# Kernel tuning notes

Measured on AMD Instinct MI355X. Metric: run time of the kernel, lower is better.

The kernel has to match this reference:

```python
import jax, jax.numpy as jnp
import numpy as np

B, T, C = 1, 2048, 2048
N_HEAD, N_KV = 32, 8
HD = C // N_HEAD            # 64
N_REP = N_HEAD // N_KV      # 4
WINDOW = 512                # sliding_window
N_GLOBAL = 16               # n_global_tokens


def setup_inputs() -> dict:
    key = jax.random.key(0)
    ks = jax.random.split(key, 5)
    x = jax.random.normal(ks[0], (B, T, C), jnp.float32)
    # standard RoPE frequency tables, shape (T, HD//2)
    inv_freq = 1.0 / (10000.0 ** (np.arange(0, HD, 2, dtype=np.float32) / HD))
    ang = np.outer(np.arange(T, dtype=np.float32), inv_freq)
    freqs_cos = jnp.asarray(np.cos(ang), jnp.float32)
    freqs_sin = jnp.asarray(np.sin(ang), jnp.float32)
    s = 0.02
    wq = jax.random.normal(ks[1], (C, C), jnp.float32) * s
    wk = jax.random.normal(ks[2], (N_KV * HD, C), jnp.float32) * s
    wv = jax.random.normal(ks[3], (N_KV * HD, C), jnp.float32) * s
    wo = jax.random.normal(ks[4], (C, C), jnp.float32) * s
    return {"x": x, "freqs_cos": freqs_cos, "freqs_sin": freqs_sin,
            "wq": wq, "wk": wk, "wv": wv, "wo": wo}


def _apply_rope(xh, fc, fs):
    # xh: (B, H, T, HD); fc/fs: (T, HD//2) broadcast over (B, H)
    xr = xh.reshape(*xh.shape[:-1], HD // 2, 2)
    x0, x1 = xr[..., 0], xr[..., 1]
    fc = fc[None, None]
    fs = fs[None, None]
    out = jnp.stack([x0 * fc - x1 * fs, x0 * fs + x1 * fc], axis=-1)
    return out.reshape(xh.shape)


def reference(x, freqs_cos, freqs_sin, wq, wk, wv, wo):
    Bx, Tx, Cx = x.shape
    q = (x @ wq.T).reshape(Bx, Tx, N_HEAD, HD).transpose(0, 2, 1, 3)   # (B,Hq,T,hd)
    k = (x @ wk.T).reshape(Bx, Tx, N_KV, HD).transpose(0, 2, 1, 3)     # (B,Hkv,T,hd)
    v = (x @ wv.T).reshape(Bx, Tx, N_KV, HD).transpose(0, 2, 1, 3)
    q = _apply_rope(q, freqs_cos, freqs_sin)
    k = _apply_rope(k, freqs_cos, freqs_sin)

    # GQA: group query heads over shared kv heads instead of repeat_kv
    qg = q.reshape(Bx, N_KV, N_REP, Tx, HD)
    scale = 1.0 / float(np.sqrt(HD))
    scores = jnp.einsum('bgrqd,bgkd->bgrqk', qg, k) * scale  # (B,G,R,T,T)

    # sliding-window causal mask with global tokens (kv_cache=None branch)
    q_pos = jnp.arange(Tx)[:, None]
    k_pos = jnp.arange(Tx)[None, :]
    mask = (k_pos <= q_pos) & (k_pos >= q_pos - (WINDOW - 1))
    mask = mask | (k_pos < N_GLOBAL)
    # note: global columns combined with causal rows always leave >=1 valid key
    scores = jnp.where(mask[None, None, None], scores, -jnp.inf)
    probs = jax.nn.softmax(scores, axis=-1)

    y = jnp.einsum('bgrqk,bgkd->bgrqd', probs, v)
    y = y.reshape(Bx, N_HEAD, Tx, HD).transpose(0, 2, 1, 3).reshape(Bx, Tx, Cx)
    return y @ wo.T  # dropout p=0 in eval
```

## Files before the change

### kernel.cpp

```cpp
#include <hip/hip_runtime.h>
#include <hip/hip_bf16.h>

using short4v = __attribute__((ext_vector_type(4))) short;
using short8 = __attribute__((ext_vector_type(8))) short;
using f32x4  = __attribute__((ext_vector_type(4))) float;
using f32x16 = __attribute__((ext_vector_type(16))) float;
using int4v  = __attribute__((ext_vector_type(4))) int;

#define T_SEQ  2048
#define C_DIM  2048
#define NH     32
#define NKV    8
#define HD     64
#define WINDOW 512
#define NGLOB  16
#define KLOG   0.180336880f

__device__ inline ushort f2bf(float f) {
  union { float f; unsigned u; } v; v.f = f;
  unsigned u = v.u;
  u += 0x7fffu + ((u >> 16) & 1u);
  return (ushort)(u >> 16);
}
__device__ inline float bf2f(ushort h) {
  union { unsigned u; float f; } v; v.u = ((unsigned)h) << 16;
  return v.f;
}
__device__ inline float max3f(float a, float b, float c) { return fmaxf(fmaxf(a, b), c); }

__device__ __forceinline__ void gl_lds16(const ushort* g, ushort* l) {
  __builtin_amdgcn_global_load_lds(
      (const __attribute__((address_space(1))) void*)g,
      (__attribute__((address_space(3))) void*)l, 16, 0, 0);
}

__device__ __forceinline__ f32x16 zero16() {
  f32x16 v;
#pragma unroll
  for (int i = 0; i < 16; i++) v[i] = 0.f;
  return v;
}

__device__ __forceinline__ short8 cvt8(f32x4 a, f32x4 b) {
  unsigned w0, w1, w2, w3;
  asm("v_cvt_pk_bf16_f32 %0, %1, %2" : "=v"(w0) : "v"(a[0]), "v"(a[1]));
  asm("v_cvt_pk_bf16_f32 %0, %1, %2" : "=v"(w1) : "v"(a[2]), "v"(a[3]));
  asm("v_cvt_pk_bf16_f32 %0, %1, %2" : "=v"(w2) : "v"(b[0]), "v"(b[1]));
  asm("v_cvt_pk_bf16_f32 %0, %1, %2" : "=v"(w3) : "v"(b[2]), "v"(b[3]));
  int4v w = { (int)w0, (int)w1, (int)w2, (int)w3 };
  return __builtin_bit_cast(short8, w);
}

__global__ void cvt_all(const float* __restrict__ s0, ushort* __restrict__ d0, int n0,
                        const float* __restrict__ s1, ushort* __restrict__ d1, int n1,
                        const float* __restrict__ s2, ushort* __restrict__ d2, int n2,
                        const float* __restrict__ s3, ushort* __restrict__ d3, int n3,
                        const float* __restrict__ s4, ushort* __restrict__ d4, int n4) {
  int total = n0 + n1 + n2 + n3 + n4;
  int stride = gridDim.x * blockDim.x;
  for (int i = blockIdx.x * blockDim.x + threadIdx.x; i < total; i += stride) {
    int j = i; const float* s; ushort* d;
    if (j < n0) { s = s0; d = d0; }
    else { j -= n0;
      if (j < n1) { s = s1; d = d1; }
      else { j -= n1;
        if (j < n2) { s = s2; d = d2; }
        else { j -= n2;
          if (j < n3) { s = s3; d = d3; }
          else { j -= n3; s = s4; d = d4; } } } }
    f32x4 a = *reinterpret_cast<const f32x4*>(s + (size_t)j * 8);
    f32x4 b = *reinterpret_cast<const f32x4*>(s + (size_t)j * 8 + 4);
    *reinterpret_cast<short8*>(d + (size_t)j * 8) = cvt8(a, b);
  }
}

template <int MODE>
__global__ __launch_bounds__(256) void gemm2p(const ushort* __restrict__ A,
                                              const ushort* __restrict__ B0,
                                              const ushort* __restrict__ B1,
                                              const ushort* __restrict__ B2,
                                              void* __restrict__ C0,
                                              void* __restrict__ C1,
                                              void* __restrict__ C2,
                                              const float* __restrict__ fc,
                                              const float* __restrict__ fs,
                                              int K) {
  __shared__ ushort As[2][2][128][32];
  __shared__ ushort Bs[2][2][64][32];
  const int tid  = threadIdx.x;
  const int lane = tid & 63;
  const int wid  = tid >> 6;
  const int wr = wid >> 1, wc = wid & 1;
  const int r16 = lane & 15, g16 = (lane >> 4) & 3;

  int id = blockIdx.x + blockIdx.y * gridDim.x;
  int c8 = id & 7, rr = id >> 3;
  int bx, by;
  if constexpr (MODE == 1) { bx = (c8 & 3) * 12 + (rr % 12); by = (c8 >> 2) * 8 + rr / 12; }
  else                     { bx = (c8 & 3) * 8  + (rr % 8);  by = (c8 >> 2) * 8 + rr / 8; }

  const ushort* Brow;
  void* Cout;
  int ldc, col0;
  bool vtr = false;
  if constexpr (MODE == 1) {
    if (bx < 32)      { Brow = B0 + (size_t)bx * 64 * K;        Cout = C0; ldc = 2048; col0 = bx * 64; }
    else if (bx < 40) { Brow = B1 + (size_t)(bx - 32) * 64 * K; Cout = C1; ldc = 512;  col0 = (bx - 32) * 64; }
    else              { Brow = B2 + (size_t)(bx - 40) * 64 * K; Cout = C2; ldc = 512;  col0 = (bx - 40) * 64; vtr = true; }
  } else {
    Brow = B0 + (size_t)bx * 64 * K; Cout = C0; ldc = 2048; col0 = bx * 64;
  }
  const ushort* Arow = A + (size_t)by * 128 * K;

  f32x4 acc[4][2];
#pragma unroll
  for (int i = 0; i < 4; i++)
#pragma unroll
    for (int j = 0; j < 2; j++) acc[i][j] = (f32x4){0.f, 0.f, 0.f, 0.f};

  const int srow = tid >> 2, scch = tid & 3;
  const int ssc  = scch ^ ((srow >> 1) & 3);
  const int rchunk = (g16 ^ ((r16 >> 1) & 3)) * 8;

  const int nt = K >> 6;
  int d = 0;

#define STAGE(dd, k0)                                                               \
  {                                                                                 \
    gl_lds16(&Arow[(size_t)srow * K + (k0) + ssc * 8],             &As[dd][0][srow][scch * 8]);      \
    gl_lds16(&Arow[(size_t)(srow + 64) * K + (k0) + ssc * 8],      &As[dd][0][srow + 64][scch * 8]); \
    gl_lds16(&Arow[(size_t)srow * K + (k0) + 32 + ssc * 8],        &As[dd][1][srow][scch * 8]);      \
    gl_lds16(&Arow[(size_t)(srow + 64) * K + (k0) + 32 + ssc * 8], &As[dd][1][srow + 64][scch * 8]); \
    gl_lds16(&Brow[(size_t)srow * K + (k0) + ssc * 8],             &Bs[dd][0][srow][scch * 8]);      \
    gl_lds16(&Brow[(size_t)srow * K + (k0) + 32 + ssc * 8],        &Bs[dd][1][srow][scch * 8]);      \
  }

  STAGE(0, 0);
  __syncthreads();

  for (int t = 0; t < nt; ++t) {
    if (t + 1 < nt) STAGE(d ^ 1, (t + 1) * 64);
#pragma unroll
    for (int kk = 0; kk < 2; kk++) {
      short8 af[4], bfv[2];
#pragma unroll
      for (int i = 0; i < 4; i++)
        af[i] = *reinterpret_cast<const short8*>(&As[d][kk][wr * 64 + i * 16 + r16][rchunk]);
#pragma unroll
      for (int j = 0; j < 2; j++)
        bfv[j] = *reinterpret_cast<const short8*>(&Bs[d][kk][wc * 32 + j * 16 + r16][rchunk]);
#pragma unroll
      for (int i = 0; i < 4; i++)
#pragma unroll
        for (int j = 0; j < 2; j++)
          acc[i][j] = __builtin_amdgcn_mfma_f32_16x16x32_bf16(af[i], bfv[j], acc[i][j], 0, 0, 0);
    }
    __syncthreads();
    d ^= 1;
  }
#undef STAGE

  const bool doRope = (MODE == 1) && !vtr;
  const float ksc = (MODE == 1 && bx < 32) ? KLOG : 1.0f;

#pragma unroll
  for (int i = 0; i < 4; i++)
#pragma unroll
    for (int j = 0; j < 2; j++) {
      int col = col0 + wc * 32 + j * 16 + r16;
      int row0 = by * 128 + wr * 64 + i * 16 + g16 * 4;
      if (MODE == 1 && vtr) {
        short4v tv;
#pragma unroll
        for (int r = 0; r < 4; r++) tv[r] = (short)f2bf(acc[i][j][r]);
        *reinterpret_cast<short4v*>(&((ushort*)Cout)[(size_t)col * T_SEQ + row0]) = tv;
      } else if (doRope) {
        int pr = (col & 63) >> 1;
        bool ev = ((col & 1) == 0);
#pragma unroll
        for (int r = 0; r < 4; r++) {
          float a = acc[i][j][r];
          float b = __shfl_xor(a, 1);
          int t = row0 + r;
          float cv = fc[t * 32 + pr], sv = fs[t * 32 + pr];
          float v = ev ? (a * cv - b * sv) : (b * sv + a * cv);
          ((ushort*)Cout)[(size_t)t * ldc + col] = f2bf(v * ksc);
        }
      } else {
#pragma unroll
        for (int r = 0; r < 4; r++) {
          if constexpr (MODE == 0) ((float*)Cout)[(size_t)(row0 + r) * ldc + col] = acc[i][j][r];
          else                     ((ushort*)Cout)[(size_t)(row0 + r) * ldc + col] = f2bf(acc[i][j][r]);
        }
      }
    }
}

__global__ __launch_bounds__(512) void attn32(const ushort* __restrict__ Q,
                                              const ushort* __restrict__ K,
                                              const ushort* __restrict__ Vt,
                                              ushort* __restrict__ Y) {
  __shared__ ushort Klds[2][2][2048];
  __shared__ ushort Vlds[2][2][2048];
  __shared__ float oS[4][64][33];
  __shared__ float mS[4][32];
  __shared__ float sS[4][64];
  ushort (*Ot)[32][72] = reinterpret_cast<ushort (*)[32][72]>(&oS[0][0][0]);
  const int tid  = threadIdx.x;
  const int lane = tid & 63;
  const int wv   = tid >> 6;
  const int hh   = wv & 3;
  const int split = wv >> 2;
  const int g  = blockIdx.x & 7;
  const int qt = 63 - (blockIdx.x >> 3);
  const int h  = g * 4 + hh;
  const int q0 = qt << 5;
  const int l31 = lane & 31, hi = lane >> 5;
  const int hi8 = hi << 3, hi4 = hi << 2;
  const int qrow = q0 + l31;

  short8 qf[4];
#pragma unroll
  for (int s = 0; s < 4; s++)
    qf[s] = *reinterpret_cast<const short8*>(&Q[(size_t)qrow * C_DIM + h * HD + s * 16 + hi8]);

  f32x16 o[2] = { zero16(), zero16() };
  f32x16 sacc = zero16();
  float mrow = -1e30f;
  short8 ones8;
#pragma unroll
  for (int s = 0; s < 8; s++) ones8[s] = (short)0x3F80;

  auto pack8 = [&](const float* pp) -> short8 {
    unsigned wA, wB, wC, wD;
    asm("v_cvt_pk_bf16_f32 %0, %1, %2" : "=v"(wA) : "v"(pp[0]), "v"(pp[1]));
    asm("v_cvt_pk_bf16_f32 %0, %1, %2" : "=v"(wB) : "v"(pp[2]), "v"(pp[3]));
    asm("v_cvt_pk_bf16_f32 %0, %1, %2" : "=v"(wC) : "v"(pp[4]), "v"(pp[5]));
    asm("v_cvt_pk_bf16_f32 %0, %1, %2" : "=v"(wD) : "v"(pp[6]), "v"(pp[7]));
    asm("v_permlane32_swap_b32 %0, %1" : "+v"(wA), "+v"(wC));
    asm("v_permlane32_swap_b32 %0, %1" : "+v"(wB), "+v"(wD));
    int4v w4 = { (int)wA, (int)wB, (int)wC, (int)wD };
    return __builtin_bit_cast(short8, w4);
  };

  int wsr = (q0 - (WINDOW - 1)) >> 5;
  int wstart = (wsr < 1) ? 32 : (wsr << 5);
  int ntw = (q0 >= wstart) ? (((q0 - wstart) >> 5) + 1) : 0;
  const int NT = 1 + ntw;
  const int ihalf = (NT + 1) >> 1;

#define KBOF(i) ((i) == 0 ? 0 : wstart + ((i) - 1) * 32)
#define MSK(i)  ((i) == 0 || (KBOF(i) < q0 - 480) || (KBOF(i) == q0))

  const int sp_s = tid >> 8;
  const int kr = (tid >> 3) & 31, kc = tid & 7;
  const int vr = (tid >> 2) & 63, vc = tid & 3;
  const ushort* ksrc0 = K + (size_t)kr * (NKV * HD) + g * HD + ((kc ^ (kr & 7)) * 8);
  const ushort* vsrc0 = Vt + (size_t)(g * HD + vr) * T_SEQ + ((vc ^ ((vr >> 1) & 3)) * 8);
  ushort* kdst[2] = { &Klds[sp_s][0][(tid & 255) * 8], &Klds[sp_s][1][(tid & 255) * 8] };
  ushort* vdst[2] = { &Vlds[sp_s][0][(tid & 255) * 8], &Vlds[sp_s][1][(tid & 255) * 8] };

#define STAGE(dd, i0t, i1t)                                                    \
  {                                                                            \
    int idxs = sp_s ? (i1t) : (i0t);                                           \
    if (idxs > NT - 1) idxs = NT - 1;                                          \
    int kbs = KBOF(idxs);                                                      \
    gl_lds16(ksrc0 + (size_t)kbs * (NKV * HD), kdst[dd]);                      \
    gl_lds16(vsrc0 + kbs, vdst[dd]);                                           \
  }

#define PROCESS(dd, kb, domask)                                                    \
  {                                                                                \
    short8 kf0 = *reinterpret_cast<const short8*>(                                 \
        &Klds[split][dd][l31 * 64 + (((0 * 2 + hi) ^ (l31 & 7)) * 8)]);            \
    short8 kf1 = *reinterpret_cast<const short8*>(                                 \
        &Klds[split][dd][l31 * 64 + (((1 * 2 + hi) ^ (l31 & 7)) * 8)]);            \
    short8 kf2 = *reinterpret_cast<const short8*>(                                 \
        &Klds[split][dd][l31 * 64 + (((2 * 2 + hi) ^ (l31 & 7)) * 8)]);            \
    short8 kf3 = *reinterpret_cast<const short8*>(                                 \
        &Klds[split][dd][l31 * 64 + (((3 * 2 + hi) ^ (l31 & 7)) * 8)]);            \
    f32x16 sa = zero16();                                                          \
    __builtin_amdgcn_s_setprio(1);                                                 \
    sa = __builtin_amdgcn_mfma_f32_32x32x16_bf16(kf0, qf[0], sa, 0, 0, 0);         \
    sa = __builtin_amdgcn_mfma_f32_32x32x16_bf16(kf1, qf[1], sa, 0, 0, 0);         \
    sa = __builtin_amdgcn_mfma_f32_32x32x16_bf16(kf2, qf[2], sa, 0, 0, 0);         \
    sa = __builtin_amdgcn_mfma_f32_32x32x16_bf16(kf3, qf[3], sa, 0, 0, 0);         \
    __builtin_amdgcn_s_setprio(0);                                                 \
    float p[16];                                                                   \
    _Pragma("unroll") for (int r = 0; r < 16; r++) p[r] = sa[r];                   \
    if (domask) {                                                                  \
      _Pragma("unroll") for (int r = 0; r < 16; r++) {                             \
        int kidx = (kb) + (r & 3) + 8 * (r >> 2) + hi4;                            \
        bool ok = ((kidx <= qrow) && (kidx >= qrow - (WINDOW - 1))) || (kidx < NGLOB); \
        p[r] = ok ? p[r] : -1e30f;                                                 \
      }                                                                            \
    }                                                                              \
    float m0 = max3f(p[0], p[1], p[2]);                                            \
    float m1 = max3f(p[3], p[4], p[5]);                                            \
    float m2 = max3f(p[6], p[7], p[8]);                                            \
    float m3 = max3f(p[9], p[10], p[11]);                                          \
    float m4 = max3f(p[12], p[13], p[14]);                                         \
    float tmax = fmaxf(max3f(m0, m1, m2), max3f(m3, m4, p[15]));                   \
    float pmax = fmaxf(tmax, __shfl_xor(tmax, 32));                                \
    if (!__all(pmax <= mrow + 8.0f)) {                                             \
      float mnew = fmaxf(mrow, pmax);                                              \
      float corr = exp2f(mrow - mnew);                                             \
      sacc[0] *= corr;                                                             \
      _Pragma("unroll") for (int r = 0; r < 16; r++) { o[0][r] *= corr; o[1][r] *= corr; } \
      mrow = mnew;                                                                 \
    }                                                                              \
    _Pragma("unroll") for (int r = 0; r < 16; r++) p[r] = exp2f(p[r] - mrow);      \
    short8 pb0 = pack8(&p[0]);                                                     \
    short8 pb1 = pack8(&p[8]);                                                     \
    short8 v0 = *reinterpret_cast<const short8*>(                                  \
        &Vlds[split][dd][(0 * 32 + l31) * 32 + (((0 * 2 + hi) ^ ((l31 >> 1) & 3)) * 8)]); \
    short8 v1 = *reinterpret_cast<const short8*>(                                  \
        &Vlds[split][dd][(0 * 32 + l31) * 32 + (((1 * 2 + hi) ^ ((l31 >> 1) & 3)) * 8)]); \
    short8 v2 = *reinterpret_cast<const short8*>(                                  \
        &Vlds[split][dd][(1 * 32 + l31) * 32 + (((0 * 2 + hi) ^ (((32 + l31) >> 1) & 3)) * 8)]); \
    short8 v3 = *reinterpret_cast<const short8*>(                                  \
        &Vlds[split][dd][(1 * 32 + l31) * 32 + (((1 * 2 + hi) ^ (((32 + l31) >> 1) & 3)) * 8)]); \
    __builtin_amdgcn_s_setprio(1);                                                 \
    sacc = __builtin_amdgcn_mfma_f32_32x32x16_bf16(ones8, pb0, sacc, 0, 0, 0);     \
    sacc = __builtin_amdgcn_mfma_f32_32x32x16_bf16(ones8, pb1, sacc, 0, 0, 0);     \
    o[0] = __builtin_amdgcn_mfma_f32_32x32x16_bf16(v0, pb0, o[0], 0, 0, 0);        \
    o[0] = __builtin_amdgcn_mfma_f32_32x32x16_bf16(v1, pb1, o[0], 0, 0, 0);        \
    o[1] = __builtin_amdgcn_mfma_f32_32x32x16_bf16(v2, pb0, o[1], 0, 0, 0);        \
    o[1] = __builtin_amdgcn_mfma_f32_32x32x16_bf16(v3, pb1, o[1], 0, 0, 0);        \
    __builtin_amdgcn_s_setprio(0);                                                 \
  }

  STAGE(0, 0, ihalf);
  asm volatile("s_waitcnt vmcnt(0)" ::: "memory");
  __builtin_amdgcn_s_barrier();
  int d = 0;
  for (int it = 0; it < ihalf; ++it) {
    if (it + 1 < ihalf) {
      STAGE(d ^ 1, it + 1, ihalf + it + 1);
      asm volatile("s_waitcnt vmcnt(2)" ::: "memory");
    } else {
      asm volatile("s_waitcnt vmcnt(0)" ::: "memory");
    }
    __builtin_amdgcn_s_barrier();
    int idx = split ? (ihalf + it) : it;
    if (idx < NT) {
      int kb = KBOF(idx);
      PROCESS(d, kb, MSK(idx));
    }
    asm volatile("" ::: "memory");
    __builtin_amdgcn_s_barrier();
    d ^= 1;
  }
#undef STAGE
#undef PROCESS
#undef KBOF
#undef MSK

  float ssum = sacc[0];

  if (split == 1) {
    if (hi == 0) mS[hh][l31] = mrow;
    sS[hh][lane] = ssum;
#pragma unroll
    for (int ntl = 0; ntl < 2; ntl++)
#pragma unroll
      for (int r = 0; r < 16; r++) oS[hh][lane][ntl * 16 + r] = o[ntl][r];
  }
  __syncthreads();

  float inv = 0.f;
  if (split == 0) {
    float mB = mS[hh][l31];
    float sB = sS[hh][lane];
    float mN = fmaxf(mrow, mB);
    float cA = exp2f(mrow - mN), cB = exp2f(mB - mN);
    ssum = ssum * cA + sB * cB;
#pragma unroll
    for (int ntl = 0; ntl < 2; ntl++)
#pragma unroll
      for (int r = 0; r < 16; r++)
        o[ntl][r] = o[ntl][r] * cA + oS[hh][lane][ntl * 16 + r] * cB;
    inv = 1.0f / ssum;
  }
  __syncthreads();

  if (split == 0) {
#pragma unroll
    for (int ntl = 0; ntl < 2; ntl++)
#pragma unroll
      for (int r = 0; r < 16; r++) {
        int dim = ntl * 32 + (r & 3) + 8 * (r >> 2) + hi4;
        Ot[hh][l31][dim] = f2bf(o[ntl][r] * inv);
      }
  }
  __syncthreads();

  if (split == 0) {
    int qq = lane >> 1, hf = lane & 1;
#pragma unroll
    for (int c = 0; c < 4; c++) {
      short8 vv = *reinterpret_cast<const short8*>(&Ot[hh][qq][hf * 32 + c * 8]);
      *reinterpret_cast<short8*>(&Y[(size_t)(q0 + qq) * C_DIM + h * HD + hf * 32 + c * 8]) = vv;
    }
  }
}

extern "C" void kernel_launch(void* const* d_in, const int* in_sizes, int n_in,
                              void* d_out, int out_size, void* d_ws, size_t ws_size,
                              hipStream_t stream) {
  const float* x  = (const float*)d_in[0];
  const float* fc = (const float*)d_in[1];
  const float* fs = (const float*)d_in[2];
  const float* wq = (const float*)d_in[3];
  const float* wk = (const float*)d_in[4];
  const float* wv = (const float*)d_in[5];
  const float* wo = (const float*)d_in[6];
  float* out = (float*)d_out;

  const size_t SZ_X = (size_t)T_SEQ * C_DIM;
  const size_t SZ_W = (size_t)(NKV * HD) * C_DIM;

  ushort* xb  = (ushort*)d_ws;
  ushort* wqb = xb  + SZ_X;
  ushort* wkb = wqb + SZ_X;
  ushort* wvb = wkb + SZ_W;
  ushort* wob = wvb + SZ_W;
  ushort* Qb  = wob + SZ_X;
  ushort* Kb  = Qb  + SZ_X;
  ushort* Vt  = Kb  + SZ_W;
  ushort* Yb  = Vt  + SZ_W;

  cvt_all<<<1024, 256, 0, stream>>>(x,  xb,  (int)(SZ_X / 8),
                                    wq, wqb, (int)(SZ_X / 8),
                                    wk, wkb, (int)(SZ_W / 8),
                                    wv, wvb, (int)(SZ_W / 8),
                                    wo, wob, (int)(SZ_X / 8));

  gemm2p<1><<<dim3(48, 16), 256, 0, stream>>>(xb, wqb, wkb, wvb, Qb, Kb, Vt, fc, fs, C_DIM);

  attn32<<<512, 512, 0, stream>>>(Qb, Kb, Vt, Yb);

  gemm2p<0><<<dim3(32, 16), 256, 0, stream>>>(Yb, wob, nullptr, nullptr, out, nullptr, nullptr,
                                              fc, fs, C_DIM);
}
```

Measured before the change: 116.2 us.

## Add 128x128-tile 512-thread GEMM for output projection and double cvt grid

Replaces the 128x64-tile, 256-thread output-projection GEMM with a dedicated 128x128-tile kernel using 8 waves and 256 blocks. The larger tile is meant to raise operand reuse and cut global traffic, and each block waits on vmcnt instead of a full __syncthreads. The bf16 conversion kernel also gets twice as many blocks. The new GEMM launches only 256 blocks, which lowers the number of blocks per CU and may cost latency hiding.

```diff
diff --git a/kernel.cpp b/kernel.cpp
--- a/kernel.cpp
+++ b/kernel.cpp
@@ -95,21 +95,15 @@
 
   int id = blockIdx.x + blockIdx.y * gridDim.x;
   int c8 = id & 7, rr = id >> 3;
-  int bx, by;
-  if constexpr (MODE == 1) { bx = (c8 & 3) * 12 + (rr % 12); by = (c8 >> 2) * 8 + rr / 12; }
-  else                     { bx = (c8 & 3) * 8  + (rr % 8);  by = (c8 >> 2) * 8 + rr / 8; }
+  int bx = (c8 & 3) * 12 + (rr % 12), by = (c8 >> 2) * 8 + rr / 12;
 
   const ushort* Brow;
   void* Cout;
   int ldc, col0;
   bool vtr = false;
-  if constexpr (MODE == 1) {
-    if (bx < 32)      { Brow = B0 + (size_t)bx * 64 * K;        Cout = C0; ldc = 2048; col0 = bx * 64; }
-    else if (bx < 40) { Brow = B1 + (size_t)(bx - 32) * 64 * K; Cout = C1; ldc = 512;  col0 = (bx - 32) * 64; }
-    else              { Brow = B2 + (size_t)(bx - 40) * 64 * K; Cout = C2; ldc = 512;  col0 = (bx - 40) * 64; vtr = true; }
-  } else {
-    Brow = B0 + (size_t)bx * 64 * K; Cout = C0; ldc = 2048; col0 = bx * 64;
-  }
+  if (bx < 32)      { Brow = B0 + (size_t)bx * 64 * K;        Cout = C0; ldc = 2048; col0 = bx * 64; }
+  else if (bx < 40) { Brow = B1 + (size_t)(bx - 32) * 64 * K; Cout = C1; ldc = 512;  col0 = (bx - 32) * 64; }
+  else              { Brow = B2 + (size_t)(bx - 40) * 64 * K; Cout = C2; ldc = 512;  col0 = (bx - 40) * 64; vtr = true; }
   const ushort* Arow = A + (size_t)by * 128 * K;
 
   f32x4 acc[4][2];
@@ -160,8 +154,8 @@
   }
 #undef STAGE
 
-  const bool doRope = (MODE == 1) && !vtr;
-  const float ksc = (MODE == 1 && bx < 32) ? KLOG : 1.0f;
+  const bool doRope = !vtr;
+  const float ksc = (bx < 32) ? KLOG : 1.0f;
 
 #pragma unroll
   for (int i = 0; i < 4; i++)
@@ -169,7 +163,7 @@
     for (int j = 0; j < 2; j++) {
       int col = col0 + wc * 32 + j * 16 + r16;
       int row0 = by * 128 + wr * 64 + i * 16 + g16 * 4;
-      if (MODE == 1 && vtr) {
+      if (vtr) {
         short4v tv;
 #pragma unroll
         for (int r = 0; r < 4; r++) tv[r] = (short)f2bf(acc[i][j][r]);
@@ -186,13 +180,92 @@
           float v = ev ? (a * cv - b * sv) : (b * sv + a * cv);
           ((ushort*)Cout)[(size_t)t * ldc + col] = f2bf(v * ksc);
         }
-      } else {
-#pragma unroll
-        for (int r = 0; r < 4; r++) {
-          if constexpr (MODE == 0) ((float*)Cout)[(size_t)(row0 + r) * ldc + col] = acc[i][j][r];
-          else                     ((ushort*)Cout)[(size_t)(row0 + r) * ldc + col] = f2bf(acc[i][j][r]);
-        }
       }
+    }
+}
+
+__global__ __launch_bounds__(512) void gemm128(const ushort* __restrict__ A,
+                                               const ushort* __restrict__ B,
+                                               float* __restrict__ C,
+                                               int K) {
+  __shared__ ushort As[2][2][128][32];
+  __shared__ ushort Bs[2][2][128][32];
+  const int tid  = threadIdx.x;
+  const int lane = tid & 63;
+  const int wid  = tid >> 6;
+  const int wr = wid >> 2, wc = wid & 3;
+  const int r16 = lane & 15, g16 = (lane >> 4) & 3;
+
+  int id = blockIdx.x;
+  int c8 = id & 7, rr = id >> 3;
+  int bx = (c8 & 3) * 4 + (rr & 3), by = (c8 >> 2) * 8 + (rr >> 2);
+
+  const ushort* Arow = A + (size_t)by * 128 * K;
+  const ushort* Brow = B + (size_t)bx * 128 * K;
+
+  f32x4 acc[4][2];
+#pragma unroll
+  for (int i = 0; i < 4; i++)
+#pragma unroll
+    for (int j = 0; j < 2; j++) acc[i][j] = (f32x4){0.f, 0.f, 0.f, 0.f};
+
+  const int srow = tid >> 2, scch = tid & 3;
+  const int ssc  = scch ^ ((srow >> 1) & 3);
+  const int rchunk = (g16 ^ ((r16 >> 1) & 3)) * 8;
+
+  const int nt = K >> 6;
+  int d = 0;
+
+#define STAGE(dd, k0)                                                          \
+  {                                                                            \
+    gl_lds16(&Arow[(size_t)srow * K + (k0) + ssc * 8],      &As[dd][0][srow][scch * 8]); \
+    gl_lds16(&Arow[(size_t)srow * K + (k0) + 32 + ssc * 8], &As[dd][1][srow][scch * 8]); \
+    gl_lds16(&Brow[(size_t)srow * K + (k0) + ssc * 8],      &Bs[dd][0][srow][scch * 8]); \
+    gl_lds16(&Brow[(size_t)srow * K + (k0) + 32 + ssc * 8], &Bs[dd][1][srow][scch * 8]); \
+  }
+
+  STAGE(0, 0);
+  asm volatile("s_waitcnt vmcnt(0)" ::: "memory");
+  __builtin_amdgcn_s_barrier();
+
+  for (int t = 0; t < nt; ++t) {
+    if (t + 1 < nt) {
+      STAGE(d ^ 1, (t + 1) * 64);
+      asm volatile("s_waitcnt vmcnt(4)" ::: "memory");
+    } else {
+      asm volatile("s_waitcnt vmcnt(0)" ::: "memory");
+    }
+    __builtin_amdgcn_s_barrier();
+#pragma unroll
+    for (int kk = 0; kk < 2; kk++) {
+      short8 af[4], bfv[2];
+#pragma unroll
+      for (int i = 0; i < 4; i++)
+        af[i] = *reinterpret_cast<const short8*>(&As[d][kk][wr * 64 + i * 16 + r16][rchunk]);
+#pragma unroll
+      for (int j = 0; j < 2; j++)
+        bfv[j] = *reinterpret_cast<const short8*>(&Bs[d][kk][wc * 32 + j * 16 + r16][rchunk]);
+#pragma unroll
+      for (int i = 0; i < 4; i++)
+#pragma unroll
+        for (int j = 0; j < 2; j++)
+          acc[i][j] = __builtin_amdgcn_mfma_f32_16x16x32_bf16(af[i], bfv[j], acc[i][j], 0, 0, 0);
+    }
+    asm volatile("" ::: "memory");
+    __builtin_amdgcn_s_barrier();
+    d ^= 1;
+  }
+#undef STAGE
+
+#pragma unroll
+  for (int i = 0; i < 4; i++)
+#pragma unroll
+    for (int j = 0; j < 2; j++) {
+      int col = bx * 128 + wc * 32 + j * 16 + r16;
+      int row0 = by * 128 + wr * 64 + i * 16 + g16 * 4;
+#pragma unroll
+      for (int r = 0; r < 4; r++)
+        C[(size_t)(row0 + r) * C_DIM + col] = acc[i][j][r];
     }
 }
 
@@ -430,7 +503,7 @@
   ushort* Vt  = Kb  + SZ_W;
   ushort* Yb  = Vt  + SZ_W;
 
-  cvt_all<<<1024, 256, 0, stream>>>(x,  xb,  (int)(SZ_X / 8),
+  cvt_all<<<2048, 256, 0, stream>>>(x,  xb,  (int)(SZ_X / 8),
                                     wq, wqb, (int)(SZ_X / 8),
                                     wk, wkb, (int)(SZ_W / 8),
                                     wv, wvb, (int)(SZ_W / 8),
@@ -440,6 +513,5 @@
 
   attn32<<<512, 512, 0, stream>>>(Qb, Kb, Vt, Yb);
 
-  gemm2p<0><<<dim3(32, 16), 256, 0, stream>>>(Yb, wob, nullptr, nullptr, out, nullptr, nullptr,
-                                              fc, fs, C_DIM);
-}
+  gemm128<<<256, 512, 0, stream>>>(Yb, wob, out, C_DIM);
+}
```

Result: slower. 119.5 us (+2.8%).
